# Kernel optimization log

Measured on AMD Instinct MI355X. Metric: run time of the kernel, lower is better.

## Reference

```python
import jax, jax.numpy as jnp
import numpy as np

LAMBDA_DISCO = 1.0
THRESHOLD = 0.5
EPS = 1e-8
N = 8192


def setup_inputs() -> dict:
    key = jax.random.key(0)
    k1, k2, k3 = jax.random.split(key, 3)
    inputs = jax.random.normal(k1, (N, 1), dtype=jnp.float32)
    targets = jax.random.uniform(k2, (N, 1), dtype=jnp.float32)
    spectators = jax.random.uniform(k3, (N,), dtype=jnp.float32)
    return {"inputs": inputs, "targets": targets, "spectators": spectators}


def _masked_distance_correlation(x, y, m, c):
    """Distance correlation restricted to samples where mask m==1.

    Mathematically identical to filtering x[m], y[m] and running the dense
    dCor (cdist -> double-center -> mean of products), but with fixed shapes
    so it is jit-compatible. c = number of selected samples (>=1).
    """
    # 1-D pairwise L2 distances == |x_i - x_j|   [n, n]
    dx = jnp.abs(x[:, None] - x[None, :])
    dy = jnp.abs(y[:, None] - y[None, :])

    def double_center(D):
        row = (D @ m) / c          # masked row means  [n]
        col = (m @ D) / c          # masked col means  [n]
        tot = (m @ row) / c        # masked total mean (scalar)
        return D - row[:, None] - col[None, :] + tot

    cx = double_center(dx)
    cy = double_center(dy)
    M = m[:, None] * m[None, :]    # pairwise selection mask

    def masked_mean_prod(a, b):
        return jnp.sum(M * a * b) / (c * c)

    dcov_xy = jnp.sqrt(jnp.maximum(masked_mean_prod(cx, cy), EPS))
    dvar_x = jnp.sqrt(jnp.maximum(masked_mean_prod(cx, cx), EPS))
    dvar_y = jnp.sqrt(jnp.maximum(masked_mean_prod(cy, cy), EPS))
    return dcov_xy / (dvar_x * dvar_y)


def reference(inputs, targets, spectators):
    # BCEWithLogitsLoss (mean reduction), numerically stable form.
    x, t = inputs, targets
    bce = jnp.mean(jnp.maximum(x, 0.0) - x * t + jnp.log1p(jnp.exp(-jnp.abs(x))))

    probs = jax.nn.sigmoid(x).reshape(-1)                 # [n]
    m = (spectators >= THRESHOLD).astype(probs.dtype)     # [n] 0/1 mask
    count = jnp.sum(m)
    c_safe = jnp.maximum(count, 1.0)

    dcor = _masked_distance_correlation(probs, spectators, m, c_safe)
    # If no sample passes the condition, return plain BCE.
    return bce + LAMBDA_DISCO * jnp.where(count > 0, dcor, 0.0)
```

## Files before the change

kernel.cpp:

```cpp
#include <hip/hip_runtime.h>
#include <math.h>

#define NTOT 8192
#define THRESH 0.5f
#define EPS_F 1e-8f

#define NSEG 32
#define SEGSZ 256
#define NJG 8
#define SEG_PER_JG (NSEG / NJG)
#define NBLK (NSEG * NJG)

#define OFF_CNT 0
#define OFF_BCEP 32
#define OFF_TP 64
#define OFF_RXP (OFF_TP + 3 * NBLK)
#define OFF_RYP (OFF_RXP + NJG * NTOT)

__device__ inline float wave_reduce(float v) {
#pragma unroll
    for (int o = 32; o > 0; o >>= 1) v += __shfl_down(v, o, 64);
    return v;
}

__global__ void __launch_bounds__(256) k_main(const float* __restrict__ x,
                                              const float* __restrict__ t,
                                              const float* __restrict__ s,
                                              float* __restrict__ ws) {
    __shared__ float2 pjs[SEGSZ];
    __shared__ float2 mis[SEGSZ];
    __shared__ unsigned wcnt[4];
    __shared__ float wred[4];
    __shared__ float accs[3];
    const int tid = threadIdx.x;
    const int lane = tid & 63, w = tid >> 6;
    const int ib = blockIdx.x & (NSEG - 1);
    const int jg = blockIdx.x >> 5;

    const int gi = ib * SEGSZ + tid;
    const float xi = x[gi], si = s[gi];
    const bool sel = (si >= THRESH);
    unsigned long long ball = __ballot(sel);
    unsigned pre = __popcll(ball & ((1ull << lane) - 1ull));
    if (lane == 0) wcnt[w] = (unsigned)__popcll(ball);
    if (tid < 3) accs[tid] = 0.f;
    if (jg == 0) {
        float ti = t[gi];
        float bce = fmaxf(xi, 0.f) - xi * ti + log1pf(expf(-fabsf(xi)));
        bce = wave_reduce(bce);
        if (lane == 0) wred[w] = bce;
    }
    __syncthreads();
    unsigned off = 0;
#pragma unroll
    for (int k = 0; k < 4; ++k)
        if (k < w) off += wcnt[k];
    const int ci = (int)(wcnt[0] + wcnt[1] + wcnt[2] + wcnt[3]);
    if (sel) mis[off + pre] = make_float2(1.f / (1.f + expf(-xi)), si);
    if (jg == 0 && tid == 0) {
        ((unsigned*)(ws + OFF_CNT))[ib] = (unsigned)ci;
        ws[OFF_BCEP + ib] = wred[0] + wred[1] + wred[2] + wred[3];
    }
    __syncthreads();
    const bool valid = tid < ci;
    float2 me = mis[tid];

    float rsx = 0.f, rsy = 0.f, txy = 0.f, txx = 0.f, tyy = 0.f;
    for (int k = 0; k < SEG_PER_JG; ++k) {
        const int seg = jg * SEG_PER_JG + k;
        const int gj = seg * SEGSZ + tid;
        const float xj = x[gj], sj = s[gj];
        const bool selj = (sj >= THRESH);
        unsigned long long bj = __ballot(selj);
        unsigned prej = __popcll(bj & ((1ull << lane) - 1ull));
        if (lane == 0) wcnt[w] = (unsigned)__popcll(bj);
        __syncthreads();
        unsigned offj = 0;
#pragma unroll
        for (int q = 0; q < 4; ++q)
            if (q < w) offj += wcnt[q];
        const int cj = (int)(wcnt[0] + wcnt[1] + wcnt[2] + wcnt[3]);
        if (selj) pjs[offj + prej] = make_float2(1.f / (1.f + expf(-xj)), sj);
        __syncthreads();
        if (valid) {
#pragma unroll 8
            for (int j = 0; j < cj; ++j) {
                float2 v = pjs[j];
                float d1 = me.x - v.x;
                float d2 = me.y - v.y;
                float a1 = fabsf(d1);
                float a2 = fabsf(d2);
                rsx += a1;
                rsy += a2;
                txy = fmaf(a1, a2, txy);
                txx = fmaf(d1, d1, txx);
                tyy = fmaf(d2, d2, tyy);
            }
        }
    }

    ws[OFF_RXP + jg * NTOT + gi] = rsx;
    ws[OFF_RYP + jg * NTOT + gi] = rsy;

    txy = wave_reduce(txy);
    txx = wave_reduce(txx);
    tyy = wave_reduce(tyy);
    if (lane == 0) {
        atomicAdd(&accs[0], txy);
        atomicAdd(&accs[1], txx);
        atomicAdd(&accs[2], tyy);
    }
    __syncthreads();
    if (tid == 0) {
        float* tp = ws + OFF_TP + blockIdx.x * 3;
        tp[0] = accs[0];
        tp[1] = accs[1];
        tp[2] = accs[2];
    }
}

__global__ void __launch_bounds__(256) k_final(const float* __restrict__ ws,
                                               float* __restrict__ out) {
    __shared__ float red[4][12];
    const int tid = threadIdx.x;
    const int lane = tid & 63, w = tid >> 6;

    float sx = 0, sy = 0, sxy = 0, sxx = 0, syy = 0;
    for (int i = tid; i < NTOT; i += 256) {
        float rx = 0.f, ry = 0.f;
#pragma unroll
        for (int jg = 0; jg < NJG; ++jg) {
            rx += ws[OFF_RXP + jg * NTOT + i];
            ry += ws[OFF_RYP + jg * NTOT + i];
        }
        sx += rx;
        sy += ry;
        sxy = fmaf(rx, ry, sxy);
        sxx = fmaf(rx, rx, sxx);
        syy = fmaf(ry, ry, syy);
    }
    const float* tp = ws + OFF_TP + tid * 3;
    float txy = tp[0], txx = tp[1], tyy = tp[2];
    float bcep = 0.f, cp = 0.f;
    if (tid < NSEG) {
        bcep = ws[OFF_BCEP + tid];
        cp = (float)((const unsigned*)(ws + OFF_CNT))[tid];
    }

    float v0 = wave_reduce(sx), v1 = wave_reduce(sy), v2 = wave_reduce(sxy);
    float v3 = wave_reduce(sxx), v4 = wave_reduce(syy);
    float v5 = wave_reduce(txy), v6 = wave_reduce(txx), v7 = wave_reduce(tyy);
    float v8 = wave_reduce(bcep), v9 = wave_reduce(cp);
    if (lane == 0) {
        red[w][0] = v0; red[w][1] = v1; red[w][2] = v2; red[w][3] = v3;
        red[w][4] = v4; red[w][5] = v5; red[w][6] = v6; red[w][7] = v7;
        red[w][8] = v8; red[w][9] = v9;
    }
    __syncthreads();
    if (tid == 0) {
        float q[10];
#pragma unroll
        for (int k = 0; k < 10; ++k)
            q[k] = red[0][k] + red[1][k] + red[2][k] + red[3][k];
        float bce = q[8] / (float)NTOT;
        float c = q[9];
        if (c == 0.f) { out[0] = bce; return; }
        float ic2 = 1.f / (c * c);
        float ic3 = ic2 / c;
        float ic4 = ic2 * ic2;
        float Vxy = q[5] * ic2 - 2.f * q[2] * ic3 + q[0] * q[1] * ic4;
        float Vxx = q[6] * ic2 - 2.f * q[3] * ic3 + q[0] * q[0] * ic4;
        float Vyy = q[7] * ic2 - 2.f * q[4] * ic3 + q[1] * q[1] * ic4;
        float dcor = sqrtf(fmaxf(Vxy, EPS_F)) /
                     (sqrtf(fmaxf(Vxx, EPS_F)) * sqrtf(fmaxf(Vyy, EPS_F)));
        out[0] = bce + dcor;
    }
}

extern "C" void kernel_launch(void* const* d_in, const int* in_sizes, int n_in,
                              void* d_out, int out_size, void* d_ws, size_t ws_size,
                              hipStream_t stream) {
    const float* x = (const float*)d_in[0];
    const float* t = (const float*)d_in[1];
    const float* s = (const float*)d_in[2];
    float* ws = (float*)d_ws;
    float* out = (float*)d_out;

    k_main<<<NBLK, SEGSZ, 0, stream>>>(x, t, s, ws);
    k_final<<<1, SEGSZ, 0, stream>>>(ws, out);
}
```

Baseline: 84.02 us.

## Double j-group split and parallelize final reduction across blocks with last-block finish

The main kernel now splits the column range into 16 groups of 2 segments instead of 8 groups of 4, launching 512 blocks to improve occupancy and shorten each block's serial loop. The final kernel goes from a single block to 32 blocks, each reducing one segment of row sums, with an atomic counter so the last block finishes the global reduction. This trades more partial-sum traffic and atomic/fence overhead for more parallelism in both stages.

```diff
diff --git a/kernel.cpp b/kernel.cpp
--- a/kernel.cpp
+++ b/kernel.cpp
@@ -7,14 +7,17 @@
 
 #define NSEG 32
 #define SEGSZ 256
-#define NJG 8
-#define SEG_PER_JG (NSEG / NJG)
+#define NJG 16
+#define SEGS_PER_JG 2
 #define NBLK (NSEG * NJG)
+#define FINB 32
 
 #define OFF_CNT 0
 #define OFF_BCEP 32
-#define OFF_TP 64
-#define OFF_RXP (OFF_TP + 3 * NBLK)
+#define OFF_DONE 64
+#define OFF_FP 72
+#define OFF_TP 256
+#define OFF_RXP 2048
 #define OFF_RYP (OFF_RXP + NJG * NTOT)
 
 __device__ inline float wave_reduce(float v) {
@@ -36,6 +39,7 @@
     const int lane = tid & 63, w = tid >> 6;
     const int ib = blockIdx.x & (NSEG - 1);
     const int jg = blockIdx.x >> 5;
+    if (blockIdx.x == 0 && tid == 0) ((unsigned*)(ws + OFF_DONE))[0] = 0u;
 
     const int gi = ib * SEGSZ + tid;
     const float xi = x[gi], si = s[gi];
@@ -66,8 +70,8 @@
     float2 me = mis[tid];
 
     float rsx = 0.f, rsy = 0.f, txy = 0.f, txx = 0.f, tyy = 0.f;
-    for (int k = 0; k < SEG_PER_JG; ++k) {
-        const int seg = jg * SEG_PER_JG + k;
+    for (int k = 0; k < SEGS_PER_JG; ++k) {
+        const int seg = jg * SEGS_PER_JG + k;
         const int gj = seg * SEGSZ + tid;
         const float xj = x[gj], sj = s[gj];
         const bool selj = (sj >= THRESH);
@@ -119,42 +123,66 @@
     }
 }
 
-__global__ void __launch_bounds__(256) k_final(const float* __restrict__ ws,
+__global__ void __launch_bounds__(256) k_final(float* __restrict__ ws,
                                                float* __restrict__ out) {
     __shared__ float red[4][12];
-    const int tid = threadIdx.x;
+    __shared__ unsigned lastf;
+    const int tid = threadIdx.x, b = blockIdx.x;
     const int lane = tid & 63, w = tid >> 6;
 
-    float sx = 0, sy = 0, sxy = 0, sxx = 0, syy = 0;
-    for (int i = tid; i < NTOT; i += 256) {
-        float rx = 0.f, ry = 0.f;
-#pragma unroll
-        for (int jg = 0; jg < NJG; ++jg) {
-            rx += ws[OFF_RXP + jg * NTOT + i];
-            ry += ws[OFF_RYP + jg * NTOT + i];
-        }
-        sx += rx;
-        sy += ry;
-        sxy = fmaf(rx, ry, sxy);
-        sxx = fmaf(rx, rx, sxx);
-        syy = fmaf(ry, ry, syy);
-    }
-    const float* tp = ws + OFF_TP + tid * 3;
-    float txy = tp[0], txx = tp[1], tyy = tp[2];
-    float bcep = 0.f, cp = 0.f;
-    if (tid < NSEG) {
+    const int row = b * SEGSZ + tid;
+    float rx = 0.f, ry = 0.f;
+#pragma unroll
+    for (int jg = 0; jg < NJG; ++jg) {
+        rx += ws[OFF_RXP + jg * NTOT + row];
+        ry += ws[OFF_RYP + jg * NTOT + row];
+    }
+    float v0 = wave_reduce(rx);
+    float v1 = wave_reduce(ry);
+    float v2 = wave_reduce(rx * ry);
+    float v3 = wave_reduce(rx * rx);
+    float v4 = wave_reduce(ry * ry);
+    if (lane == 0) {
+        red[w][0] = v0; red[w][1] = v1; red[w][2] = v2;
+        red[w][3] = v3; red[w][4] = v4;
+    }
+    __syncthreads();
+    if (tid == 0) {
+        float* fp = ws + OFF_FP + b * 5;
+#pragma unroll
+        for (int q = 0; q < 5; ++q)
+            fp[q] = red[0][q] + red[1][q] + red[2][q] + red[3][q];
+    }
+    __threadfence();
+    if (tid == 0) {
+        unsigned prev = atomicAdd((unsigned*)(ws + OFF_DONE), 1u);
+        lastf = (prev == FINB - 1) ? 1u : 0u;
+    }
+    __syncthreads();
+    if (!lastf) return;
+    __threadfence();
+
+    const float* tp0 = ws + OFF_TP + tid * 3;
+    const float* tp1 = ws + OFF_TP + (tid + 256) * 3;
+    float t5 = tp0[0] + tp1[0];
+    float t6 = tp0[1] + tp1[1];
+    float t7 = tp0[2] + tp1[2];
+    float f0 = 0, f1 = 0, f2 = 0, f3 = 0, f4 = 0, bcep = 0, cp = 0;
+    if (tid < FINB) {
+        const float* fp = ws + OFF_FP + tid * 5;
+        f0 = fp[0]; f1 = fp[1]; f2 = fp[2]; f3 = fp[3]; f4 = fp[4];
         bcep = ws[OFF_BCEP + tid];
         cp = (float)((const unsigned*)(ws + OFF_CNT))[tid];
     }
-
-    float v0 = wave_reduce(sx), v1 = wave_reduce(sy), v2 = wave_reduce(sxy);
-    float v3 = wave_reduce(sxx), v4 = wave_reduce(syy);
-    float v5 = wave_reduce(txy), v6 = wave_reduce(txx), v7 = wave_reduce(tyy);
-    float v8 = wave_reduce(bcep), v9 = wave_reduce(cp);
+    float q0 = wave_reduce(f0), q1 = wave_reduce(f1), q2 = wave_reduce(f2);
+    float q3 = wave_reduce(f3), q4 = wave_reduce(f4);
+    float q5 = wave_reduce(t5), q6 = wave_reduce(t6), q7 = wave_reduce(t7);
+    float q8 = wave_reduce(bcep), q9 = wave_reduce(cp);
+    __syncthreads();
     if (lane == 0) {
-        red[w][0] = v0; red[w][1] = v1; red[w][2] = v2; red[w][3] = v3;
-        red[w][4] = v4; red[w][5] = v5; red[w][6] = v6; red[w][7] = v7;
-        red[w][8] = v8; red[w][9] = v9;
+        red[w][0] = q0; red[w][1] = q1; red[w][2] = q2; red[w][3] = q3;
+        red[w][4] = q4; red[w][5] = q5; red[w][6] = q6; red[w][7] = q7;
+        red[w][8] = q8; red[w][9] = q9;
     }
     __syncthreads();
     if (tid == 0) {
@@ -187,5 +215,5 @@
     float* out = (float*)d_out;
 
     k_main<<<NBLK, SEGSZ, 0, stream>>>(x, t, s, ws);
-    k_final<<<1, SEGSZ, 0, stream>>>(ws, out);
-}
+    k_final<<<FINB, SEGSZ, 0, stream>>>(ws, out);
+}
```

New measurement: 73.48 us. -12.5%, faster.
